# Performance work log

Measured on AMD Instinct MI355X. Metric: run time of the kernel, lower is better.

## Reference

```python
import jax, jax.numpy as jnp
import numpy as np

MARGIN = 0.25
GAMMA = 256.0
NEG_INF = -1e30


def setup_inputs() -> dict:
    key = jax.random.key(0)
    k1, k2 = jax.random.split(key)
    B, D = 8192, 128
    return {
        "embeddings_a": jax.random.normal(k1, (B, D), dtype=jnp.float32),
        "embeddings_b": jax.random.normal(k2, (B, D), dtype=jnp.float32),
    }


def _l2_normalize(x, eps=1e-12):
    # matches F.normalize(p=2, dim=1): x / max(||x||, eps)
    n = jnp.sqrt(jnp.sum(x * x, axis=1, keepdims=True))
    return x / jnp.maximum(n, eps)


def reference(embeddings_a, embeddings_b):
    B = embeddings_a.shape[0]
    a = _l2_normalize(embeddings_a)
    b = _l2_normalize(embeddings_b)
    sim = a @ b.T  # [B, B]

    pos_mask = jnp.eye(B, dtype=bool)  # labels=None path

    # positive logits: -gamma * relu((1-m) - s) * (s - m)
    logit_pos = -GAMMA * jnp.maximum((1.0 - MARGIN) - sim, 0.0) * (sim - MARGIN)
    # negative logits:  gamma * relu(s - m) * (s + m)
    logit_neg = GAMMA * jnp.maximum(sim - MARGIN, 0.0) * (sim + MARGIN)

    # masked per-row logsumexp over positive / negative sets
    lse_pos = jax.nn.logsumexp(jnp.where(pos_mask, logit_pos, NEG_INF), axis=1)
    lse_neg = jax.nn.logsumexp(jnp.where(pos_mask, NEG_INF, logit_neg), axis=1)

    losses = jax.nn.softplus(lse_pos + lse_neg)  # [B]
    return jnp.mean(losses)  # reduction='mean'
```

## Files before the change

### kernel.cpp

```cpp
#include <hip/hip_runtime.h>


#define B_N 8192
#define D_K 128
#define MARGIN 0.25f
#define M2 (MARGIN * MARGIN)
#define GAMMA 256.0f

#define BM 128
#define BN 128
#define NCH 8
#define CPB (B_N / NCH)
#define NSUB (CPB / BN)

typedef __attribute__((ext_vector_type(8))) short short8;
typedef __attribute__((ext_vector_type(4))) float f32x4;

__device__ __forceinline__ unsigned short f2bf(float x) {
  unsigned u = __float_as_uint(x);
  u += 0x7FFFu + ((u >> 16) & 1u);
  return (unsigned short)(u >> 16);
}

__device__ __forceinline__ void gload_lds16(const void* gsrc, void* ldst) {
  __builtin_amdgcn_global_load_lds(
      (const __attribute__((address_space(1))) void*)gsrc,
      (__attribute__((address_space(3))) void*)ldst, 16, 0, 0);
}

__global__ __launch_bounds__(256) void norm_diag_kernel(
    const float* __restrict__ a, const float* __restrict__ b,
    unsigned short* __restrict__ abf, unsigned short* __restrict__ bbf,
    float* __restrict__ diag) {
  int wave = threadIdx.x >> 6, lane = threadIdx.x & 63;
  int r = blockIdx.x * 4 + wave;
  int half = lane >> 5, l32 = lane & 31;
  const float* src = half ? b : a;
  unsigned short* dst = half ? bbf : abf;

  float4 v = ((const float4*)(src + (size_t)r * D_K))[l32];
  float ss = v.x * v.x + v.y * v.y + v.z * v.z + v.w * v.w;
  #pragma unroll
  for (int m = 16; m >= 1; m >>= 1) ss += __shfl_xor(ss, m);
  float inv = 1.0f / fmaxf(sqrtf(ss), 1e-12f);
  float n0 = v.x * inv, n1 = v.y * inv, n2 = v.z * inv, n3 = v.w * inv;

  ushort4 o = {f2bf(n0), f2bf(n1), f2bf(n2), f2bf(n3)};
  ((ushort4*)(dst + (size_t)r * D_K))[l32] = o;

  float d = n0 * __shfl_xor(n0, 32) + n1 * __shfl_xor(n1, 32) +
            n2 * __shfl_xor(n2, 32) + n3 * __shfl_xor(n3, 32);
  #pragma unroll
  for (int m = 16; m >= 1; m >>= 1) d += __shfl_xor(d, m);
  if (lane == 0) diag[r] = d;
}

__global__ __launch_bounds__(256, 2) void simlse_kernel(
    const unsigned short* __restrict__ abf, const unsigned short* __restrict__ bbf,
    float* __restrict__ partS) {
  __shared__ __align__(16) unsigned short L[2][BM * D_K];
  __shared__ float sred[BM][2];

  const int tid = threadIdx.x;
  const int wave = tid >> 6, lane = tid & 63;
  const int r16 = lane & 15, kq = lane >> 4;
  const int wr = wave >> 1, wc = wave & 1;
  const int rowBase = blockIdx.y * BM;
  const int chunk = blockIdx.x;

  #pragma unroll
  for (int it = 0; it < 8; ++it) {
    int gb = it * 256 + wave * 64;
    int g = gb + lane;
    int row = g >> 4, sl = g & 15;
    int sls = sl ^ (row & 7);
    gload_lds16(abf + (size_t)(rowBase + row) * D_K + sls * 8, &L[0][gb * 8]);
  }
  {
    const int colBase = chunk * CPB;
    #pragma unroll
    for (int it = 0; it < 8; ++it) {
      int gb = it * 256 + wave * 64;
      int g = gb + lane;
      int row = g >> 4, sl = g & 15;
      int sls = sl ^ (row & 7);
      gload_lds16(bbf + (size_t)(colBase + row) * D_K + sls * 8, &L[1][gb * 8]);
    }
  }
  __syncthreads();

  short8 af[4][4];
  #pragma unroll
  for (int mi = 0; mi < 4; ++mi) {
    int row = wr * 64 + mi * 16 + r16;
    #pragma unroll
    for (int ks = 0; ks < 4; ++ks) {
      int slot = (ks * 4 + kq) ^ (row & 7);
      af[mi][ks] = *(const short8*)&L[0][row * D_K + slot * 8];
    }
  }
  __syncthreads();

  {
    const int colBase = chunk * CPB + BN;
    #pragma unroll
    for (int it = 0; it < 8; ++it) {
      int gb = it * 256 + wave * 64;
      int g = gb + lane;
      int row = g >> 4, sl = g & 15;
      int sls = sl ^ (row & 7);
      gload_lds16(bbf + (size_t)(colBase + row) * D_K + sls * 8, &L[0][gb * 8]);
    }
  }

  float Ssum[4][4];
  #pragma unroll
  for (int mi = 0; mi < 4; ++mi)
    #pragma unroll
    for (int r = 0; r < 4; ++r) Ssum[mi][r] = 0.0f;

  #pragma unroll 2
  for (int st = 0; st < NSUB; ++st) {
    const unsigned short* cb = L[(st + 1) & 1];

    f32x4 acc[4][4];
    const f32x4 z4 = {0.f, 0.f, 0.f, 0.f};
    #pragma unroll
    for (int mi = 0; mi < 4; ++mi)
      #pragma unroll
      for (int ni = 0; ni < 4; ++ni) acc[mi][ni] = z4;

    #pragma unroll
    for (int ks = 0; ks < 4; ++ks) {
      short8 bf[4];
      #pragma unroll
      for (int ni = 0; ni < 4; ++ni) {
        int row = wc * 64 + ni * 16 + r16;
        int slot = (ks * 4 + kq) ^ (row & 7);
        bf[ni] = *(const short8*)&cb[row * D_K + slot * 8];
      }
      #pragma unroll
      for (int mi = 0; mi < 4; ++mi)
        #pragma unroll
        for (int ni = 0; ni < 4; ++ni)
          acc[mi][ni] = __builtin_amdgcn_mfma_f32_16x16x32_bf16(
              af[mi][ks], bf[ni], acc[mi][ni], 0, 0, 0);
    }

    #pragma unroll
    for (int mi = 0; mi < 4; ++mi)
      #pragma unroll
      for (int ni = 0; ni < 4; ++ni) {
        f32x4 v = acc[mi][ni];
        float mx = fmaxf(fmaxf(v[0], v[1]), fmaxf(v[2], v[3]));
        if (__any(mx > MARGIN)) {
          #pragma unroll
          for (int r = 0; r < 4; ++r) {
            float s = v[r];
            float t = fmaf(s, s, -M2);
            float z = (s > MARGIN) ? GAMMA * t : 0.0f;
            Ssum[mi][r] += __expf(z) - 1.0f;
          }
        }
      }

    __syncthreads();

    if (st + 2 < NSUB) {
      const int colBase = chunk * CPB + (st + 2) * BN;
      #pragma unroll
      for (int it = 0; it < 8; ++it) {
        int gb = it * 256 + wave * 64;
        int g = gb + lane;
        int row = g >> 4, sl = g & 15;
        int sls = sl ^ (row & 7);
        gload_lds16(bbf + (size_t)(colBase + row) * D_K + sls * 8,
                    &((unsigned short*)L[(st + 1) & 1])[gb * 8]);
      }
    }
  }

  #pragma unroll
  for (int mi = 0; mi < 4; ++mi)
    #pragma unroll
    for (int r = 0; r < 4; ++r) {
      float v = Ssum[mi][r];
      v += __shfl_xor(v, 1);
      v += __shfl_xor(v, 2);
      v += __shfl_xor(v, 4);
      v += __shfl_xor(v, 8);
      if (r16 == 0) sred[wr * 64 + mi * 16 + kq * 4 + r][wc] = v;
    }
  __syncthreads();
  if (tid < BM)
    partS[(size_t)chunk * B_N + rowBase + tid] = sred[tid][0] + sred[tid][1];
}

__global__ __launch_bounds__(256) void rowfin_kernel(
    const float* __restrict__ partS, const float* __restrict__ diag,
    float* __restrict__ bpart) {
  __shared__ float red[256];
  int i = blockIdx.x * 256 + threadIdx.x;
  float S = 0.0f;
  #pragma unroll
  for (int c = 0; c < NCH; ++c) S += partS[(size_t)c * B_N + i];
  float sd = diag[i];
  float td = fmaf(sd, sd, -M2);
  float zd = (sd > MARGIN) ? GAMMA * td : 0.0f;
  float ed = __expf(zd);
  float lneg = __logf((float)B_N + S - ed);
  float lpos = -GAMMA * fmaxf((1.0f - MARGIN) - sd, 0.0f) * (sd - MARGIN);
  float x = lpos + lneg;
  float loss = fmaxf(x, 0.0f) + log1pf(__expf(-fabsf(x)));
  red[threadIdx.x] = loss;
  __syncthreads();
  #pragma unroll
  for (int s = 128; s >= 1; s >>= 1) {
    if (threadIdx.x < s) red[threadIdx.x] += red[threadIdx.x + s];
    __syncthreads();
  }
  if (threadIdx.x == 0) bpart[blockIdx.x] = red[0];
}

__global__ __launch_bounds__(64) void mean_kernel(
    const float* __restrict__ bpart, float* __restrict__ out) {
  int lane = threadIdx.x;
  float v = (lane < 32) ? bpart[lane] : 0.0f;
  #pragma unroll
  for (int m = 32; m >= 1; m >>= 1) v += __shfl_xor(v, m);
  if (lane == 0) out[0] = v * (1.0f / B_N);
}

extern "C" void kernel_launch(void* const* d_in, const int* in_sizes, int n_in,
                              void* d_out, int out_size, void* d_ws, size_t ws_size,
                              hipStream_t stream) {
  const float* a = (const float*)d_in[0];
  const float* b = (const float*)d_in[1];
  float* out = (float*)d_out;

  char* w = (char*)d_ws;
  unsigned short* abf = (unsigned short*)w;
  unsigned short* bbf = (unsigned short*)(w + (size_t)B_N * D_K * 2);
  float* partS = (float*)(w + (size_t)B_N * D_K * 4);
  float* diag = partS + (size_t)NCH * B_N;
  float* bpart = diag + B_N;

  norm_diag_kernel<<<B_N / 4, 256, 0, stream>>>(a, b, abf, bbf, diag);
  simlse_kernel<<<dim3(NCH, B_N / BM), 256, 0, stream>>>(abf, bbf, partS);
  rowfin_kernel<<<B_N / 256, 256, 0, stream>>>(partS, diag, bpart);
  mean_kernel<<<1, 64, 0, stream>>>(bpart, out);
}
```

Measured before the change: 41.23 us.

## Switch to 32x32x16 MFMA tiles, set wave priority, merge final reduction kernels

Result: slower. 49.71 us (+20.6%).

```diff
diff --git a/kernel.cpp b/kernel.cpp
--- a/kernel.cpp
+++ b/kernel.cpp
@@ -14,7 +14,7 @@
 #define NSUB (CPB / BN)
 
 typedef __attribute__((ext_vector_type(8))) short short8;
-typedef __attribute__((ext_vector_type(4))) float f32x4;
+typedef __attribute__((ext_vector_type(16))) float f32x16;
 
 __device__ __forceinline__ unsigned short f2bf(float x) {
   unsigned u = __float_as_uint(x);
@@ -63,103 +63,107 @@
 
   const int tid = threadIdx.x;
   const int wave = tid >> 6, lane = tid & 63;
-  const int r16 = lane & 15, kq = lane >> 4;
+  const int l31 = lane & 31, h = lane >> 5;
   const int wr = wave >> 1, wc = wave & 1;
   const int rowBase = blockIdx.y * BM;
   const int chunk = blockIdx.x;
 
+  int stageOff[8];
   #pragma unroll
   for (int it = 0; it < 8; ++it) {
-    int gb = it * 256 + wave * 64;
-    int g = gb + lane;
+    int g = it * 256 + wave * 64 + lane;
     int row = g >> 4, sl = g & 15;
-    int sls = sl ^ (row & 7);
-    gload_lds16(abf + (size_t)(rowBase + row) * D_K + sls * 8, &L[0][gb * 8]);
-  }
+    stageOff[it] = row * D_K + (sl ^ (row & 7)) * 8;
+  }
+
   {
-    const int colBase = chunk * CPB;
+    const unsigned short* srcA = abf + (size_t)rowBase * D_K;
+    const unsigned short* srcB = bbf + (size_t)(chunk * CPB) * D_K;
     #pragma unroll
     for (int it = 0; it < 8; ++it) {
       int gb = it * 256 + wave * 64;
-      int g = gb + lane;
-      int row = g >> 4, sl = g & 15;
-      int sls = sl ^ (row & 7);
-      gload_lds16(bbf + (size_t)(colBase + row) * D_K + sls * 8, &L[1][gb * 8]);
-    }
-  }
-  __syncthreads();
-
-  short8 af[4][4];
-  #pragma unroll
-  for (int mi = 0; mi < 4; ++mi) {
-    int row = wr * 64 + mi * 16 + r16;
-    #pragma unroll
-    for (int ks = 0; ks < 4; ++ks) {
-      int slot = (ks * 4 + kq) ^ (row & 7);
-      af[mi][ks] = *(const short8*)&L[0][row * D_K + slot * 8];
-    }
-  }
-  __syncthreads();
-
-  {
-    const int colBase = chunk * CPB + BN;
+      gload_lds16(srcA + stageOff[it], &L[0][gb * 8]);
+    }
     #pragma unroll
     for (int it = 0; it < 8; ++it) {
       int gb = it * 256 + wave * 64;
-      int g = gb + lane;
-      int row = g >> 4, sl = g & 15;
-      int sls = sl ^ (row & 7);
-      gload_lds16(bbf + (size_t)(colBase + row) * D_K + sls * 8, &L[0][gb * 8]);
-    }
-  }
-
-  float Ssum[4][4];
-  #pragma unroll
-  for (int mi = 0; mi < 4; ++mi)
-    #pragma unroll
-    for (int r = 0; r < 4; ++r) Ssum[mi][r] = 0.0f;
+      gload_lds16(srcB + stageOff[it], &L[1][gb * 8]);
+    }
+  }
+  __syncthreads();
+
+  short8 af[2][8];
+  #pragma unroll
+  for (int mi = 0; mi < 2; ++mi) {
+    int rowA = wr * 64 + mi * 32 + l31;
+    #pragma unroll
+    for (int ksp = 0; ksp < 8; ++ksp) {
+      int slot = (ksp * 2 + h) ^ (rowA & 7);
+      af[mi][ksp] = *(const short8*)&L[0][rowA * D_K + slot * 8];
+    }
+  }
+  __syncthreads();
+
+  {
+    const unsigned short* srcB = bbf + (size_t)(chunk * CPB + BN) * D_K;
+    #pragma unroll
+    for (int it = 0; it < 8; ++it) {
+      int gb = it * 256 + wave * 64;
+      gload_lds16(srcB + stageOff[it], &L[0][gb * 8]);
+    }
+  }
+
+  float Ssum[2][16];
+  #pragma unroll
+  for (int mi = 0; mi < 2; ++mi)
+    #pragma unroll
+    for (int r = 0; r < 16; ++r) Ssum[mi][r] = 0.0f;
+
+  const int rowB0 = wc * 64 + l31;
+  const int rowB1 = wc * 64 + 32 + l31;
 
   #pragma unroll 2
   for (int st = 0; st < NSUB; ++st) {
     const unsigned short* cb = L[(st + 1) & 1];
 
-    f32x4 acc[4][4];
-    const f32x4 z4 = {0.f, 0.f, 0.f, 0.f};
-    #pragma unroll
-    for (int mi = 0; mi < 4; ++mi)
+    f32x16 acc[2][2];
+    #pragma unroll
+    for (int mi = 0; mi < 2; ++mi)
       #pragma unroll
-      for (int ni = 0; ni < 4; ++ni) acc[mi][ni] = z4;
-
-    #pragma unroll
-    for (int ks = 0; ks < 4; ++ks) {
-      short8 bf[4];
+      for (int ni = 0; ni < 2; ++ni)
+        #pragma unroll
+        for (int r = 0; r < 16; ++r) acc[mi][ni][r] = 0.0f;
+
+    __builtin_amdgcn_s_setprio(1);
+    #pragma unroll
+    for (int ksp = 0; ksp < 8; ++ksp) {
+      int slot0 = (ksp * 2 + h) ^ (rowB0 & 7);
+      int slot1 = (ksp * 2 + h) ^ (rowB1 & 7);
+      short8 bf0 = *(const short8*)&cb[rowB0 * D_K + slot0 * 8];
+      short8 bf1 = *(const short8*)&cb[rowB1 * D_K + slot1 * 8];
+      acc[0][0] = __builtin_amdgcn_mfma_f32_32x32x16_bf16(af[0][ksp], bf0, acc[0][0], 0, 0, 0);
+      acc[0][1] = __builtin_amdgcn_mfma_f32_32x32x16_bf16(af[0][ksp], bf1, acc[0][1], 0, 0, 0);
+      acc[1][0] = __builtin_amdgcn_mfma_f32_32x32x16_bf16(af[1][ksp], bf0, acc[1][0], 0, 0, 0);
+      acc[1][1] = __builtin_amdgcn_mfma_f32_32x32x16_bf16(af[1][ksp], bf1, acc[1][1], 0, 0, 0);
+    }
+    __builtin_amdgcn_s_setprio(0);
+
+    #pragma unroll
+    for (int mi = 0; mi < 2; ++mi)
       #pragma unroll
-      for (int ni = 0; ni < 4; ++ni) {
-        int row = wc * 64 + ni * 16 + r16;
-        int slot = (ks * 4 + kq) ^ (row & 7);
-        bf[ni] = *(const short8*)&cb[row * D_K + slot * 8];
-      }
-      #pragma unroll
-      for (int mi = 0; mi < 4; ++mi)
+      for (int ni = 0; ni < 2; ++ni) {
+        const f32x16 v = acc[mi][ni];
         #pragma unroll
-        for (int ni = 0; ni < 4; ++ni)
-          acc[mi][ni] = __builtin_amdgcn_mfma_f32_16x16x32_bf16(
-              af[mi][ks], bf[ni], acc[mi][ni], 0, 0, 0);
-    }
-
-    #pragma unroll
-    for (int mi = 0; mi < 4; ++mi)
-      #pragma unroll
-      for (int ni = 0; ni < 4; ++ni) {
-        f32x4 v = acc[mi][ni];
-        float mx = fmaxf(fmaxf(v[0], v[1]), fmaxf(v[2], v[3]));
-        if (__any(mx > MARGIN)) {
-          #pragma unroll
-          for (int r = 0; r < 4; ++r) {
-            float s = v[r];
-            float t = fmaf(s, s, -M2);
-            float z = (s > MARGIN) ? GAMMA * t : 0.0f;
-            Ssum[mi][r] += __expf(z) - 1.0f;
+        for (int q = 0; q < 4; ++q) {
+          float mx = fmaxf(fmaxf(v[q * 4 + 0], v[q * 4 + 1]),
+                           fmaxf(v[q * 4 + 2], v[q * 4 + 3]));
+          if (__any(mx > MARGIN)) {
+            #pragma unroll
+            for (int t = 0; t < 4; ++t) {
+              float s = v[q * 4 + t];
+              float z = (s > MARGIN) ? GAMMA * fmaf(s, s, -M2) : 0.0f;
+              Ssum[mi][q * 4 + t] += __expf(z) - 1.0f;
+            }
           }
         }
       }
@@ -167,68 +171,65 @@
     __syncthreads();
 
     if (st + 2 < NSUB) {
-      const int colBase = chunk * CPB + (st + 2) * BN;
+      const unsigned short* srcB =
+          bbf + (size_t)(chunk * CPB + (st + 2) * BN) * D_K;
+      unsigned short* dstB = (unsigned short*)L[(st + 1) & 1];
       #pragma unroll
       for (int it = 0; it < 8; ++it) {
         int gb = it * 256 + wave * 64;
-        int g = gb + lane;
-        int row = g >> 4, sl = g & 15;
-        int sls = sl ^ (row & 7);
-        gload_lds16(bbf + (size_t)(colBase + row) * D_K + sls * 8,
-                    &((unsigned short*)L[(st + 1) & 1])[gb * 8]);
+        gload_lds16(srcB + stageOff[it], &dstB[gb * 8]);
       }
     }
   }
 
   #pragma unroll
-  for (int mi = 0; mi < 4; ++mi)
-    #pragma unroll
-    for (int r = 0; r < 4; ++r) {
-      float v = Ssum[mi][r];
+  for (int mi = 0; mi < 2; ++mi)
+    #pragma unroll
+    for (int rg = 0; rg < 16; ++rg) {
+      float v = Ssum[mi][rg];
       v += __shfl_xor(v, 1);
       v += __shfl_xor(v, 2);
       v += __shfl_xor(v, 4);
       v += __shfl_xor(v, 8);
-      if (r16 == 0) sred[wr * 64 + mi * 16 + kq * 4 + r][wc] = v;
+      v += __shfl_xor(v, 16);
+      if (l31 == 0) {
+        int lr = wr * 64 + mi * 32 + (rg & 3) + 8 * (rg >> 2) + 4 * h;
+        sred[lr][wc] = v;
+      }
     }
   __syncthreads();
   if (tid < BM)
     partS[(size_t)chunk * B_N + rowBase + tid] = sred[tid][0] + sred[tid][1];
 }
 
-__global__ __launch_bounds__(256) void rowfin_kernel(
+__global__ __launch_bounds__(1024) void final_kernel(
     const float* __restrict__ partS, const float* __restrict__ diag,
-    float* __restrict__ bpart) {
-  __shared__ float red[256];
-  int i = blockIdx.x * 256 + threadIdx.x;
-  float S = 0.0f;
-  #pragma unroll
-  for (int c = 0; c < NCH; ++c) S += partS[(size_t)c * B_N + i];
-  float sd = diag[i];
-  float td = fmaf(sd, sd, -M2);
-  float zd = (sd > MARGIN) ? GAMMA * td : 0.0f;
-  float ed = __expf(zd);
-  float lneg = __logf((float)B_N + S - ed);
-  float lpos = -GAMMA * fmaxf((1.0f - MARGIN) - sd, 0.0f) * (sd - MARGIN);
-  float x = lpos + lneg;
-  float loss = fmaxf(x, 0.0f) + log1pf(__expf(-fabsf(x)));
-  red[threadIdx.x] = loss;
-  __syncthreads();
-  #pragma unroll
-  for (int s = 128; s >= 1; s >>= 1) {
-    if (threadIdx.x < s) red[threadIdx.x] += red[threadIdx.x + s];
-    __syncthreads();
-  }
-  if (threadIdx.x == 0) bpart[blockIdx.x] = red[0];
-}
-
-__global__ __launch_bounds__(64) void mean_kernel(
-    const float* __restrict__ bpart, float* __restrict__ out) {
-  int lane = threadIdx.x;
-  float v = (lane < 32) ? bpart[lane] : 0.0f;
-  #pragma unroll
-  for (int m = 32; m >= 1; m >>= 1) v += __shfl_xor(v, m);
-  if (lane == 0) out[0] = v * (1.0f / B_N);
+    float* __restrict__ out) {
+  __shared__ float red[16];
+  int tid = threadIdx.x, lane = tid & 63, wid = tid >> 6;
+  float acc = 0.0f;
+  for (int i = tid; i < B_N; i += 1024) {
+    float S = 0.0f;
+    #pragma unroll
+    for (int c = 0; c < NCH; ++c) S += partS[(size_t)c * B_N + i];
+    float sd = diag[i];
+    float zd = (sd > MARGIN) ? GAMMA * fmaf(sd, sd, -M2) : 0.0f;
+    float ed = __expf(zd);
+    float lneg = __logf((float)B_N + S - ed);
+    float lpos = -GAMMA * fmaxf((1.0f - MARGIN) - sd, 0.0f) * (sd - MARGIN);
+    float x = lpos + lneg;
+    acc += fmaxf(x, 0.0f) + log1pf(__expf(-fabsf(x)));
+  }
+  #pragma unroll
+  for (int m = 32; m >= 1; m >>= 1) acc += __shfl_xor(acc, m);
+  if (lane == 0) red[wid] = acc;
+  __syncthreads();
+  if (tid == 0) {
+    float t = 0.0f;
+    #pragma unroll
+    for (int i = 0; i < 16; ++i) t += red[i];
+    out[0] = t * (1.0f / B_N);
+  }
 }
 
 extern "C" void kernel_launch(void* const* d_in, const int* in_sizes, int n_in,
@@ -243,10 +244,8 @@
   unsigned short* bbf = (unsigned short*)(w + (size_t)B_N * D_K * 2);
   float* partS = (float*)(w + (size_t)B_N * D_K * 4);
   float* diag = partS + (size_t)NCH * B_N;
-  float* bpart = diag + B_N;
 
   norm_diag_kernel<<<B_N / 4, 256, 0, stream>>>(a, b, abf, bbf, diag);
   simlse_kernel<<<dim3(NCH, B_N / BM), 256, 0, stream>>>(abf, bbf, partS);
-  rowfin_kernel<<<B_N / 256, 256, 0, stream>>>(partS, diag, bpart);
-  mean_kernel<<<1, 64, 0, stream>>>(bpart, out);
-}
+  final_kernel<<<1, 1024, 0, stream>>>(partS, diag, out);
+}
```
